# Kernel optimization log

Measured on AMD Instinct MI355X. Metric: run time of the kernel, lower is better.

## Reference

```python
import jax, jax.numpy as jnp
import numpy as np

D = 1024
H = 16
DH = D // H
F = 4096
EPS = 1e-5

def layernorm(x, gamma, beta):
    mean = jnp.mean(x, axis=-1, keepdims=True)
    var = jnp.mean((x - mean) ** 2, axis=-1, keepdims=True)  # biased variance
    return gamma * (x - mean) / jnp.sqrt(var + EPS) + beta

def setup_inputs() -> dict:
    key = jax.random.key(0)
    ks = jax.random.split(key, 12)
    s = 1.0 / np.sqrt(D)
    sf = 1.0 / np.sqrt(F)
    return {
        "x": jax.random.normal(ks[0], (16, 512, D), dtype=jnp.float32),
        "Wq": jax.random.normal(ks[1], (H, D, DH), dtype=jnp.float32) * s,
        "Wk": jax.random.normal(ks[2], (H, D, DH), dtype=jnp.float32) * s,
        "Wv": jax.random.normal(ks[3], (H, D, DH), dtype=jnp.float32) * s,
        "Wo": jax.random.normal(ks[4], (D, D), dtype=jnp.float32) * s,
        "bo": jax.random.normal(ks[5], (D,), dtype=jnp.float32) * s,
        "gamma1": jnp.ones((D,), dtype=jnp.float32),
        "beta1": jnp.zeros((D,), dtype=jnp.float32),
        "gamma2": jnp.ones((D,), dtype=jnp.float32),
        "beta2": jnp.zeros((D,), dtype=jnp.float32),
        "W1": jax.random.normal(ks[6], (D, F), dtype=jnp.float32) * s,
        "b1": jax.random.normal(ks[7], (F,), dtype=jnp.float32) * s,
        "W2": jax.random.normal(ks[8], (F, D), dtype=jnp.float32) * sf,
        "b2": jax.random.normal(ks[9], (D,), dtype=jnp.float32) * sf,
    }

def reference(x, Wq, Wk, Wv, Wo, bo, gamma1, beta1, gamma2, beta2, W1, b1, W2, b2):
    B, S, _ = x.shape
    n1 = layernorm(x, gamma1, beta1)
    # per-head projections (no bias) -> [B,H,S,DH]
    Q = jnp.einsum('bsd,hde->bhse', n1, Wq)
    K = jnp.einsum('bsd,hde->bhse', n1, Wk)
    V = jnp.einsum('bsd,hde->bhse', n1, Wv)
    scores = jnp.einsum('bhse,bhte->bhst', Q, K) / jnp.sqrt(jnp.float32(DH))
    causal = jnp.tril(jnp.ones((S, S), dtype=bool))  # keep lower triangle
    scores = jnp.where(causal, scores, -jnp.inf)
    attn = jax.nn.softmax(scores, axis=-1)  # dropout is identity at eval
    heads = jnp.einsum('bhst,bhte->bhse', attn, V)
    concat = heads.transpose(0, 2, 1, 3).reshape(B, S, D)  # concat heads in order
    x = x + (concat @ Wo + bo)
    n2 = layernorm(x, gamma2, beta2)
    ff = jax.nn.gelu(n2 @ W1 + b1, approximate=False) @ W2 + b2
    return x + ff
```

## Files before the change

### kernel.cpp

```cpp
#include <hip/hip_runtime.h>
#include <hip/hip_bf16.h>
#include <math.h>

constexpr int Dm = 1024;
constexpr int Hh = 16;
constexpr int Ff = 4096;
constexpr int Ss = 512;
constexpr int Bbatch = 16;
constexpr int NT = Bbatch * Ss;
constexpr float EPSc = 1e-5f;

typedef __attribute__((ext_vector_type(8))) short bfrag;
typedef __attribute__((ext_vector_type(4))) float f32x4;

static __device__ __forceinline__ float gelu_f(float v) {
    return 0.5f * v * (1.0f + erff(v * 0.70710678118654752f));
}

static __device__ __forceinline__ void gload16(const void* g, void* l) {
    __builtin_amdgcn_global_load_lds((__attribute__((address_space(1))) void*)g,
                                     (__attribute__((address_space(3))) void*)l,
                                     16, 0, 0);
}

#define SWZ(row, colb) ((row) * 128 + ((colb) ^ (((row) & 7) << 4)))

__global__ void __launch_bounds__(256) transpose_cvt(const float* __restrict__ in,
                                                     __hip_bfloat16* __restrict__ out,
                                                     int R, int C,
                                                     long in_zs, long out_zs) {
    __shared__ float tile[32][33];
    const float* inz = in + (size_t)blockIdx.z * in_zs;
    __hip_bfloat16* outz = out + (size_t)blockIdx.z * out_zs;
    const int c0 = blockIdx.x * 32, r0 = blockIdx.y * 32;
    const int tx = threadIdx.x & 31, ty4 = (threadIdx.x >> 5) * 4;
    #pragma unroll
    for (int i = 0; i < 4; i++)
        tile[ty4 + i][tx] = inz[(size_t)(r0 + ty4 + i) * C + c0 + tx];
    __syncthreads();
    #pragma unroll
    for (int i = 0; i < 4; i++)
        outz[(size_t)(c0 + ty4 + i) * R + r0 + tx] = __float2bfloat16(tile[tx][ty4 + i]);
}

__global__ void __launch_bounds__(256) ln_bf16(const float* __restrict__ x,
                                               const float* __restrict__ gamma,
                                               const float* __restrict__ beta,
                                               __hip_bfloat16* __restrict__ out) {
    const int row = blockIdx.x;
    const int tid = threadIdx.x;
    const int lane = tid & 63, w = tid >> 6;
    float4 xv = reinterpret_cast<const float4*>(x + (size_t)row * Dm)[tid];
    float s  = xv.x + xv.y + xv.z + xv.w;
    float ss = xv.x * xv.x + xv.y * xv.y + xv.z * xv.z + xv.w * xv.w;
    #pragma unroll
    for (int o = 32; o > 0; o >>= 1) {
        s  += __shfl_down(s,  o, 64);
        ss += __shfl_down(ss, o, 64);
    }
    __shared__ float red[2][4];
    if (lane == 0) { red[0][w] = s; red[1][w] = ss; }
    __syncthreads();
    float st  = red[0][0] + red[0][1] + red[0][2] + red[0][3];
    float sst = red[1][0] + red[1][1] + red[1][2] + red[1][3];
    float mean = st * (1.0f / Dm);
    float var  = sst * (1.0f / Dm) - mean * mean;
    float inv  = rsqrtf(var + EPSc);
    float4 g = reinterpret_cast<const float4*>(gamma)[tid];
    float4 b = reinterpret_cast<const float4*>(beta)[tid];
    __hip_bfloat16 t[4] __attribute__((aligned(8)));
    t[0] = __float2bfloat16((xv.x - mean) * inv * g.x + b.x);
    t[1] = __float2bfloat16((xv.y - mean) * inv * g.y + b.y);
    t[2] = __float2bfloat16((xv.z - mean) * inv * g.z + b.z);
    t[3] = __float2bfloat16((xv.w - mean) * inv * g.w + b.w);
    *reinterpret_cast<ushort4*>(out + (size_t)row * Dm + tid * 4) =
        *reinterpret_cast<ushort4*>(t);
}

template<int EPI>
__global__ void __launch_bounds__(256) gemm_mfma(const __hip_bfloat16* __restrict__ A, int lda,
                                                 const __hip_bfloat16* __restrict__ Bt, int ldb,
                                                 const float* __restrict__ bias,
                                                 const float* __restrict__ res,
                                                 void* __restrict__ Cout, int ldc,
                                                 int nbx, int K) {
    __shared__ __hip_bfloat16 As[128 * 32];
    __shared__ __hip_bfloat16 Bs[128 * 32];
    const int tid = threadIdx.x, l = tid & 63, w = tid >> 6;
    const int lr = l & 15, lg = l >> 4;
    const int nwg = gridDim.x, cpx = nwg >> 3;
    const int bid = blockIdx.x;
    const int sbid = (bid & 7) * cpx + (bid >> 3);
    const int bx = sbid % nbx, by = sbid / nbx;
    const int m0 = by * 128, n0 = bx * 128;
    const int wr = w >> 1, wc = w & 1;
    const int sr = l >> 2, scc = (l & 3) * 8;

    f32x4 acc[4][4] = {};
    for (int k0 = 0; k0 < K; k0 += 32) {
        #pragma unroll
        for (int j = 0; j < 2; j++) {
            const int slot = w * 2 + j;
            const int r = slot * 16 + sr;
            gload16(A  + (size_t)(m0 + r) * lda + k0 + scc, As + slot * 512);
            gload16(Bt + (size_t)(n0 + r) * ldb + k0 + scc, Bs + slot * 512);
        }
        __syncthreads();
        bfrag a[4], b[4];
        #pragma unroll
        for (int mi = 0; mi < 4; mi++)
            a[mi] = *reinterpret_cast<const bfrag*>(As + (wr * 64 + mi * 16 + lr) * 32 + lg * 8);
        #pragma unroll
        for (int ni = 0; ni < 4; ni++)
            b[ni] = *reinterpret_cast<const bfrag*>(Bs + (wc * 64 + ni * 16 + lr) * 32 + lg * 8);
        #pragma unroll
        for (int mi = 0; mi < 4; mi++)
            #pragma unroll
            for (int ni = 0; ni < 4; ni++)
                acc[mi][ni] = __builtin_amdgcn_mfma_f32_16x16x32_bf16(a[mi], b[ni], acc[mi][ni], 0, 0, 0);
        __syncthreads();
    }
    const int rb = m0 + wr * 64 + lg * 4;
    const int cb = n0 + wc * 64 + lr;
    #pragma unroll
    for (int mi = 0; mi < 4; mi++) {
        #pragma unroll
        for (int ni = 0; ni < 4; ni++) {
            #pragma unroll
            for (int rg = 0; rg < 4; rg++) {
                const int row = rb + mi * 16 + rg;
                const int col = cb + ni * 16;
                const size_t off = (size_t)row * ldc + col;
                const float v = acc[mi][ni][rg];
                if (EPI == 0) {
                    ((__hip_bfloat16*)Cout)[off] = __float2bfloat16(v);
                } else if (EPI == 1) {
                    ((float*)Cout)[off] = v + bias[col] + res[off];
                } else if (EPI == 2) {
                    ((__hip_bfloat16*)Cout)[off] = __float2bfloat16(gelu_f(v + bias[col]));
                } else {
                    ((float*)Cout)[off] = ((float*)Cout)[off] + v + bias[col];
                }
            }
        }
    }
}

__global__ void __launch_bounds__(256) attn_mfma(const __hip_bfloat16* __restrict__ QKV,
                                                 __hip_bfloat16* __restrict__ Oc) {
    constexpr int LDQ = 3072;
    __shared__ __hip_bfloat16 Qs[64 * 64];
    __shared__ __hip_bfloat16 Ks[64 * 64];
    __shared__ __hip_bfloat16 Vts[64 * 64];
    __shared__ __hip_bfloat16 Ps[4][16 * 64];
    const int tid = threadIdx.x, l = tid & 63, w = tid >> 6;
    const int lr = l & 15, lg = l >> 4;
    const int qt = blockIdx.x & 7;
    const int h  = (blockIdx.x >> 3) & 15;
    const int b  = blockIdx.x >> 7;

    const __hip_bfloat16* Qg = QKV + (size_t)(b * Ss + qt * 64) * LDQ + h * 64;
    const __hip_bfloat16* Kg = QKV + (size_t)(b * Ss) * LDQ + 1024 + h * 64;
    const __hip_bfloat16* Vg = QKV + (size_t)(b * Ss) * LDQ + 2048 + h * 64;

    const int r8 = l >> 3;
    const int scol = 8 * ((l & 7) ^ r8);

    #pragma unroll
    for (int j = 0; j < 2; j++) {
        const int slot = w * 2 + j;
        gload16(Qg + (size_t)(slot * 8 + r8) * LDQ + scol, Qs + slot * 512);
    }

    float m_run[4] = {-1e30f, -1e30f, -1e30f, -1e30f};
    float l_run[4] = {0.f, 0.f, 0.f, 0.f};
    f32x4 acc_o[4] = {};

    for (int kt = 0; kt <= qt; ++kt) {
        __syncthreads();
        #pragma unroll
        for (int j = 0; j < 2; j++) {
            const int slot = w * 2 + j;
            gload16(Kg + (size_t)(kt * 64 + slot * 8 + r8) * LDQ + scol, Ks + slot * 512);
        }
        unsigned short* vt = reinterpret_cast<unsigned short*>(Vts);
        #pragma unroll
        for (int j = 0; j < 2; j++) {
            const int e = tid + j * 256;
            const int key = e >> 3, f0 = (e & 7) * 8;
            const uint4 raw = *reinterpret_cast<const uint4*>(
                Vg + (size_t)(kt * 64 + key) * LDQ + f0);
            const unsigned int rw[4] = {raw.x, raw.y, raw.z, raw.w};
            #pragma unroll
            for (int e2 = 0; e2 < 8; e2++) {
                const int feat = f0 + e2;
                const int ad = feat * 128 + ((key * 2) ^ ((feat & 7) << 4));
                vt[ad >> 1] = (unsigned short)(rw[e2 >> 1] >> ((e2 & 1) * 16));
            }
        }
        __syncthreads();

        f32x4 s4[4] = {};
        #pragma unroll
        for (int kk = 0; kk < 2; kk++) {
            const bfrag aq = *reinterpret_cast<const bfrag*>(
                (const char*)Qs + SWZ(w * 16 + lr, kk * 64 + lg * 16));
            #pragma unroll
            for (int ni = 0; ni < 4; ni++) {
                const bfrag bk = *reinterpret_cast<const bfrag*>(
                    (const char*)Ks + SWZ(ni * 16 + lr, kk * 64 + lg * 16));
                s4[ni] = __builtin_amdgcn_mfma_f32_16x16x32_bf16(aq, bk, s4[ni], 0, 0, 0);
            }
        }
        float p[4][4];
        #pragma unroll
        for (int ni = 0; ni < 4; ni++)
            #pragma unroll
            for (int rg = 0; rg < 4; rg++)
                p[ni][rg] = s4[ni][rg] * 0.125f;
        if (kt == qt) {
            #pragma unroll
            for (int ni = 0; ni < 4; ni++)
                #pragma unroll
                for (int rg = 0; rg < 4; rg++)
                    if (ni * 16 + lr > w * 16 + lg * 4 + rg) p[ni][rg] = -1e30f;
        }
        float sf[4];
        #pragma unroll
        for (int rg = 0; rg < 4; rg++) {
            float mx = fmaxf(fmaxf(p[0][rg], p[1][rg]), fmaxf(p[2][rg], p[3][rg]));
            #pragma unroll
            for (int o = 1; o < 16; o <<= 1) mx = fmaxf(mx, __shfl_xor(mx, o, 64));
            const float mn = fmaxf(m_run[rg], mx);
            sf[rg] = __expf(m_run[rg] - mn);
            m_run[rg] = mn;
        }
        float rsum[4] = {};
        #pragma unroll
        for (int ni = 0; ni < 4; ni++)
            #pragma unroll
            for (int rg = 0; rg < 4; rg++) {
                const float e = __expf(p[ni][rg] - m_run[rg]);
                p[ni][rg] = e;
                rsum[rg] += e;
            }
        #pragma unroll
        for (int rg = 0; rg < 4; rg++) {
            #pragma unroll
            for (int o = 1; o < 16; o <<= 1) rsum[rg] += __shfl_xor(rsum[rg], o, 64);
            l_run[rg] = l_run[rg] * sf[rg] + rsum[rg];
        }
        #pragma unroll
        for (int di = 0; di < 4; di++)
            #pragma unroll
            for (int rg = 0; rg < 4; rg++)
                acc_o[di][rg] *= sf[rg];
        unsigned short* pw = reinterpret_cast<unsigned short*>(Ps[w]);
        #pragma unroll
        for (int ni = 0; ni < 4; ni++)
            #pragma unroll
            for (int rg = 0; rg < 4; rg++) {
                const int prow = lg * 4 + rg;
                const int ad = SWZ(prow, (ni * 16 + lr) * 2);
                __hip_bfloat16 pb = __float2bfloat16(p[ni][rg]);
                pw[ad >> 1] = *reinterpret_cast<unsigned short*>(&pb);
            }
        #pragma unroll
        for (int kk = 0; kk < 2; kk++) {
            const bfrag pa = *reinterpret_cast<const bfrag*>(
                (const char*)Ps[w] + SWZ(lr, kk * 64 + lg * 16));
            #pragma unroll
            for (int di = 0; di < 4; di++) {
                const bfrag vb = *reinterpret_cast<const bfrag*>(
                    (const char*)Vts + SWZ(di * 16 + lr, kk * 64 + lg * 16));
                acc_o[di] = __builtin_amdgcn_mfma_f32_16x16x32_bf16(pa, vb, acc_o[di], 0, 0, 0);
            }
        }
    }
    #pragma unroll
    for (int di = 0; di < 4; di++)
        #pragma unroll
        for (int rg = 0; rg < 4; rg++) {
            const int q = qt * 64 + w * 16 + lg * 4 + rg;
            const float v = acc_o[di][rg] / l_run[rg];
            Oc[(size_t)(b * Ss + q) * Dm + h * 64 + di * 16 + lr] = __float2bfloat16(v);
        }
}

extern "C" void kernel_launch(void* const* d_in, const int* in_sizes, int n_in,
                              void* d_out, int out_size, void* d_ws, size_t ws_size,
                              hipStream_t stream) {
    const float* x   = (const float*)d_in[0];
    const float* Wq  = (const float*)d_in[1];
    const float* Wk  = (const float*)d_in[2];
    const float* Wv  = (const float*)d_in[3];
    const float* Wo  = (const float*)d_in[4];
    const float* bo  = (const float*)d_in[5];
    const float* g1  = (const float*)d_in[6];
    const float* be1 = (const float*)d_in[7];
    const float* g2  = (const float*)d_in[8];
    const float* be2 = (const float*)d_in[9];
    const float* W1  = (const float*)d_in[10];
    const float* b1  = (const float*)d_in[11];
    const float* W2  = (const float*)d_in[12];
    const float* b2  = (const float*)d_in[13];
    float* out = (float*)d_out;

    char* wsb = (char*)d_ws;
    __hip_bfloat16* WqkvT = (__hip_bfloat16*)(wsb);
    __hip_bfloat16* WoT   = (__hip_bfloat16*)(wsb + 6291456);
    __hip_bfloat16* W1T   = (__hip_bfloat16*)(wsb + 8388608);
    __hip_bfloat16* W2T   = (__hip_bfloat16*)(wsb + 16777216);
    __hip_bfloat16* n1    = (__hip_bfloat16*)(wsb + 25165824);
    __hip_bfloat16* QKV   = (__hip_bfloat16*)(wsb + 41943040);
    __hip_bfloat16* concat = n1;
    __hip_bfloat16* n2     = n1;
    __hip_bfloat16* h1     = QKV;

    transpose_cvt<<<dim3(2, 32, 16), 256, 0, stream>>>(Wq, WqkvT,              1024, 64, 65536, 65536);
    transpose_cvt<<<dim3(2, 32, 16), 256, 0, stream>>>(Wk, WqkvT + 1024 * 1024, 1024, 64, 65536, 65536);
    transpose_cvt<<<dim3(2, 32, 16), 256, 0, stream>>>(Wv, WqkvT + 2048 * 1024, 1024, 64, 65536, 65536);
    transpose_cvt<<<dim3(32, 32, 1), 256, 0, stream>>>(Wo, WoT, 1024, 1024, 0, 0);
    transpose_cvt<<<dim3(128, 32, 1), 256, 0, stream>>>(W1, W1T, 1024, 4096, 0, 0);
    transpose_cvt<<<dim3(32, 128, 1), 256, 0, stream>>>(W2, W2T, 4096, 1024, 0, 0);

    ln_bf16<<<NT, 256, 0, stream>>>(x, g1, be1, n1);
    gemm_mfma<0><<<24 * 64, 256, 0, stream>>>(n1, Dm, WqkvT, Dm, nullptr, nullptr,
                                              QKV, 3072, 24, Dm);
    attn_mfma<<<NT * Hh / 64, 256, 0, stream>>>(QKV, concat);
    gemm_mfma<1><<<8 * 64, 256, 0, stream>>>(concat, Dm, WoT, Dm, bo, x,
                                             out, Dm, 8, Dm);
    ln_bf16<<<NT, 256, 0, stream>>>(out, g2, be2, n2);
    gemm_mfma<2><<<32 * 64, 256, 0, stream>>>(n2, Dm, W1T, Dm, b1, nullptr,
                                              h1, Ff, 32, Dm);
    gemm_mfma<3><<<8 * 64, 256, 0, stream>>>(h1, Ff, W2T, Ff, b2, nullptr,
                                             out, Dm, 8, Ff);
}
```

Measured before the change: 473.4 us.

## Replace GEMM with 256-row tiles, double-buffered LDS, swizzle and 8 waves

Replaces the 128x128, K=32 single-buffered MFMA GEMM with a 512-thread kernel using 256xBN tiles (BN 256 or 128) and K=64 steps. Two LDS buffers are loaded ahead, with explicit vmcnt waits, so global-to-LDS loads overlap the MFMA work. An XOR swizzle avoids LDS bank conflicts, and s_setprio raises wave priority around the MFMA bursts. The larger tiles cut operand refetch per FLOP but raise register and LDS use (up to 128KB LDS), which may limit occupancy; the hand-set vmcnt counts must match the number of issued loads.

Measured after the change: 503.4 us. +6.3%, slower.

```diff
diff --git a/kernel.cpp b/kernel.cpp
--- a/kernel.cpp
+++ b/kernel.cpp
@@ -77,59 +77,88 @@
         *reinterpret_cast<ushort4*>(t);
 }
 
-template<int EPI>
-__global__ void __launch_bounds__(256) gemm_mfma(const __hip_bfloat16* __restrict__ A, int lda,
-                                                 const __hip_bfloat16* __restrict__ Bt, int ldb,
-                                                 const float* __restrict__ bias,
-                                                 const float* __restrict__ res,
-                                                 void* __restrict__ Cout, int ldc,
-                                                 int nbx, int K) {
-    __shared__ __hip_bfloat16 As[128 * 32];
-    __shared__ __hip_bfloat16 Bs[128 * 32];
+template<int BN_, int EPI>
+__global__ void __launch_bounds__(512) gemm8(const __hip_bfloat16* __restrict__ A, int lda,
+                                             const __hip_bfloat16* __restrict__ Bt, int ldb,
+                                             const float* __restrict__ bias,
+                                             const float* __restrict__ res,
+                                             void* __restrict__ Cout, int ldc,
+                                             int nbx, int K) {
+    constexpr int NREP = BN_ / 64;
+    constexpr int WNS  = BN_ / 4;
+    __shared__ __hip_bfloat16 As[2][256 * 64];
+    __shared__ __hip_bfloat16 Bs[2][BN_ * 64];
     const int tid = threadIdx.x, l = tid & 63, w = tid >> 6;
     const int lr = l & 15, lg = l >> 4;
-    const int nwg = gridDim.x, cpx = nwg >> 3;
-    const int bid = blockIdx.x;
-    const int sbid = (bid & 7) * cpx + (bid >> 3);
+    const int nwg = gridDim.x;
+    const int sbid = (blockIdx.x & 7) * (nwg >> 3) + (blockIdx.x >> 3);
     const int bx = sbid % nbx, by = sbid / nbx;
-    const int m0 = by * 128, n0 = bx * 128;
-    const int wr = w >> 1, wc = w & 1;
-    const int sr = l >> 2, scc = (l & 3) * 8;
-
-    f32x4 acc[4][4] = {};
-    for (int k0 = 0; k0 < K; k0 += 32) {
-        #pragma unroll
-        for (int j = 0; j < 2; j++) {
-            const int slot = w * 2 + j;
-            const int r = slot * 16 + sr;
-            gload16(A  + (size_t)(m0 + r) * lda + k0 + scc, As + slot * 512);
-            gload16(Bt + (size_t)(n0 + r) * ldb + k0 + scc, Bs + slot * 512);
-        }
-        __syncthreads();
-        bfrag a[4], b[4];
-        #pragma unroll
-        for (int mi = 0; mi < 4; mi++)
-            a[mi] = *reinterpret_cast<const bfrag*>(As + (wr * 64 + mi * 16 + lr) * 32 + lg * 8);
-        #pragma unroll
-        for (int ni = 0; ni < 4; ni++)
-            b[ni] = *reinterpret_cast<const bfrag*>(Bs + (wc * 64 + ni * 16 + lr) * 32 + lg * 8);
-        #pragma unroll
-        for (int mi = 0; mi < 4; mi++)
-            #pragma unroll
-            for (int ni = 0; ni < 4; ni++)
-                acc[mi][ni] = __builtin_amdgcn_mfma_f32_16x16x32_bf16(a[mi], b[ni], acc[mi][ni], 0, 0, 0);
-        __syncthreads();
-    }
-    const int rb = m0 + wr * 64 + lg * 4;
-    const int cb = n0 + wc * 64 + lr;
-    #pragma unroll
-    for (int mi = 0; mi < 4; mi++) {
-        #pragma unroll
-        for (int ni = 0; ni < 4; ni++) {
+    const int m0 = by * 256, n0 = bx * BN_;
+    const int wr = w >> 2, wc = w & 3;
+    const int srow = l >> 3;
+    const int scol = ((l & 7) ^ srow) * 8;
+
+    const int NK = K >> 6;
+    auto STAGE = [&](int t, int bsel) {
+        const int k0 = t * 64;
+        #pragma unroll
+        for (int j = 0; j < 4; j++) {
+            const int rb = j * 64 + w * 8;
+            gload16(A + (size_t)(m0 + rb + srow) * lda + k0 + scol, &As[bsel][rb * 64]);
+        }
+        #pragma unroll
+        for (int j = 0; j < NREP; j++) {
+            const int rb = j * 64 + w * 8;
+            gload16(Bt + (size_t)(n0 + rb + srow) * ldb + k0 + scol, &Bs[bsel][rb * 64]);
+        }
+    };
+
+    f32x4 acc[8][NREP] = {};
+    STAGE(0, 0);
+    STAGE(1, 1);
+    for (int t = 0; t < NK; t++) {
+        const int cur = t & 1;
+        if (t + 1 < NK) {
+            if constexpr (BN_ == 256) asm volatile("s_waitcnt vmcnt(8)" ::: "memory");
+            else                      asm volatile("s_waitcnt vmcnt(6)" ::: "memory");
+        } else {
+            asm volatile("s_waitcnt vmcnt(0)" ::: "memory");
+        }
+        __builtin_amdgcn_s_barrier();
+        const char* Ab = (const char*)&As[cur][0];
+        const char* Bb = (const char*)&Bs[cur][0];
+        #pragma unroll
+        for (int kk = 0; kk < 2; kk++) {
+            bfrag a[8], b[NREP];
+            #pragma unroll
+            for (int mi = 0; mi < 8; mi++) {
+                const int row = wr * 128 + mi * 16 + lr;
+                a[mi] = *(const bfrag*)(Ab + row * 128 + ((((kk << 2) + lg) ^ (row & 7)) << 4));
+            }
+            #pragma unroll
+            for (int ni = 0; ni < NREP; ni++) {
+                const int row = wc * WNS + ni * 16 + lr;
+                b[ni] = *(const bfrag*)(Bb + row * 128 + ((((kk << 2) + lg) ^ (row & 7)) << 4));
+            }
+            __builtin_amdgcn_s_setprio(1);
+            #pragma unroll
+            for (int mi = 0; mi < 8; mi++)
+                #pragma unroll
+                for (int ni = 0; ni < NREP; ni++)
+                    acc[mi][ni] = __builtin_amdgcn_mfma_f32_16x16x32_bf16(a[mi], b[ni], acc[mi][ni], 0, 0, 0);
+            __builtin_amdgcn_s_setprio(0);
+        }
+        __builtin_amdgcn_s_barrier();
+        if (t + 2 < NK) STAGE(t + 2, cur);
+    }
+    #pragma unroll
+    for (int mi = 0; mi < 8; mi++) {
+        #pragma unroll
+        for (int ni = 0; ni < NREP; ni++) {
             #pragma unroll
             for (int rg = 0; rg < 4; rg++) {
-                const int row = rb + mi * 16 + rg;
-                const int col = cb + ni * 16;
+                const int row = m0 + wr * 128 + mi * 16 + lg * 4 + rg;
+                const int col = n0 + wc * WNS + ni * 16 + lr;
                 const size_t off = (size_t)row * ldc + col;
                 const float v = acc[mi][ni][rg];
                 if (EPI == 0) {
@@ -325,14 +354,14 @@
     transpose_cvt<<<dim3(32, 128, 1), 256, 0, stream>>>(W2, W2T, 4096, 1024, 0, 0);
 
     ln_bf16<<<NT, 256, 0, stream>>>(x, g1, be1, n1);
-    gemm_mfma<0><<<24 * 64, 256, 0, stream>>>(n1, Dm, WqkvT, Dm, nullptr, nullptr,
-                                              QKV, 3072, 24, Dm);
+    gemm8<256, 0><<<384, 512, 0, stream>>>(n1, Dm, WqkvT, Dm, nullptr, nullptr,
+                                           QKV, 3072, 12, Dm);
     attn_mfma<<<NT * Hh / 64, 256, 0, stream>>>(QKV, concat);
-    gemm_mfma<1><<<8 * 64, 256, 0, stream>>>(concat, Dm, WoT, Dm, bo, x,
-                                             out, Dm, 8, Dm);
+    gemm8<128, 1><<<256, 512, 0, stream>>>(concat, Dm, WoT, Dm, bo, x,
+                                           out, Dm, 8, Dm);
     ln_bf16<<<NT, 256, 0, stream>>>(out, g2, be2, n2);
-    gemm_mfma<2><<<32 * 64, 256, 0, stream>>>(n2, Dm, W1T, Dm, b1, nullptr,
-                                              h1, Ff, 32, Dm);
-    gemm_mfma<3><<<8 * 64, 256, 0, stream>>>(h1, Ff, W2T, Ff, b2, nullptr,
-                                             out, Dm, 8, Ff);
-}
+    gemm8<256, 2><<<512, 512, 0, stream>>>(n2, Dm, W1T, Dm, b1, nullptr,
+                                           h1, Ff, 16, Dm);
+    gemm8<128, 3><<<256, 512, 0, stream>>>(h1, Ff, W2T, Ff, b2, nullptr,
+                                           out, Dm, 8, Ff);
+}
```

## Deepen GEMM K-tile to 64 with XOR-swizzled LDS and use tanh GELU

Applied to the files above, without the earlier changes.

The GEMM kernel now stages a 128x64 K-slice per iteration instead of 128x32. This halves the number of barrier pairs per output tile. LDS rows are XOR-swizzled on the global->LDS load and on the fragment reads to avoid bank conflicts at the wider 128-byte row stride. Separately, the exact erf GELU is replaced by a tanh approximation computed with __expf, which cheapens the FFN epilogue but changes numerics versus the reference's exact GELU.

After: 425.8 us. 10.0% less time.

```diff
diff --git a/kernel.cpp b/kernel.cpp
--- a/kernel.cpp
+++ b/kernel.cpp
@@ -14,7 +14,10 @@
 typedef __attribute__((ext_vector_type(4))) float f32x4;
 
 static __device__ __forceinline__ float gelu_f(float v) {
-    return 0.5f * v * (1.0f + erff(v * 0.70710678118654752f));
+    const float u = v * (0.7978845608f + 0.0356774081f * v * v);
+    const float e = __expf(2.0f * u);
+    const float th = 1.0f - 2.0f / (e + 1.0f);
+    return 0.5f * v * (1.0f + th);
 }
 
 static __device__ __forceinline__ void gload16(const void* g, void* l) {
@@ -78,46 +81,52 @@
 }
 
 template<int EPI>
-__global__ void __launch_bounds__(256) gemm_mfma(const __hip_bfloat16* __restrict__ A, int lda,
-                                                 const __hip_bfloat16* __restrict__ Bt, int ldb,
-                                                 const float* __restrict__ bias,
-                                                 const float* __restrict__ res,
-                                                 void* __restrict__ Cout, int ldc,
-                                                 int nbx, int K) {
-    __shared__ __hip_bfloat16 As[128 * 32];
-    __shared__ __hip_bfloat16 Bs[128 * 32];
+__global__ void __launch_bounds__(256) gemm_m97(const __hip_bfloat16* __restrict__ A, int lda,
+                                                const __hip_bfloat16* __restrict__ Bt, int ldb,
+                                                const float* __restrict__ bias,
+                                                const float* __restrict__ res,
+                                                void* __restrict__ Cout, int ldc,
+                                                int nbx, int K) {
+    __shared__ __hip_bfloat16 As[128 * 64];
+    __shared__ __hip_bfloat16 Bs[128 * 64];
     const int tid = threadIdx.x, l = tid & 63, w = tid >> 6;
     const int lr = l & 15, lg = l >> 4;
-    const int nwg = gridDim.x, cpx = nwg >> 3;
-    const int bid = blockIdx.x;
-    const int sbid = (bid & 7) * cpx + (bid >> 3);
+    const int nwg = gridDim.x;
+    const int sbid = (blockIdx.x & 7) * (nwg >> 3) + (blockIdx.x >> 3);
     const int bx = sbid % nbx, by = sbid / nbx;
     const int m0 = by * 128, n0 = bx * 128;
     const int wr = w >> 1, wc = w & 1;
-    const int sr = l >> 2, scc = (l & 3) * 8;
+    const int srow = l >> 3;
+    const int scol = ((l & 7) ^ srow) * 8;
 
     f32x4 acc[4][4] = {};
-    for (int k0 = 0; k0 < K; k0 += 32) {
-        #pragma unroll
-        for (int j = 0; j < 2; j++) {
-            const int slot = w * 2 + j;
-            const int r = slot * 16 + sr;
-            gload16(A  + (size_t)(m0 + r) * lda + k0 + scc, As + slot * 512);
-            gload16(Bt + (size_t)(n0 + r) * ldb + k0 + scc, Bs + slot * 512);
+    for (int k0 = 0; k0 < K; k0 += 64) {
+        #pragma unroll
+        for (int j = 0; j < 4; j++) {
+            const int rb = w * 32 + j * 8;
+            gload16(A  + (size_t)(m0 + rb + srow) * lda + k0 + scol, As + rb * 64);
+            gload16(Bt + (size_t)(n0 + rb + srow) * ldb + k0 + scol, Bs + rb * 64);
         }
         __syncthreads();
-        bfrag a[4], b[4];
-        #pragma unroll
-        for (int mi = 0; mi < 4; mi++)
-            a[mi] = *reinterpret_cast<const bfrag*>(As + (wr * 64 + mi * 16 + lr) * 32 + lg * 8);
-        #pragma unroll
-        for (int ni = 0; ni < 4; ni++)
-            b[ni] = *reinterpret_cast<const bfrag*>(Bs + (wc * 64 + ni * 16 + lr) * 32 + lg * 8);
-        #pragma unroll
-        for (int mi = 0; mi < 4; mi++)
-            #pragma unroll
-            for (int ni = 0; ni < 4; ni++)
-                acc[mi][ni] = __builtin_amdgcn_mfma_f32_16x16x32_bf16(a[mi], b[ni], acc[mi][ni], 0, 0, 0);
+        #pragma unroll
+        for (int kk = 0; kk < 2; kk++) {
+            bfrag a[4], b[4];
+            #pragma unroll
+            for (int mi = 0; mi < 4; mi++) {
+                const int row = wr * 64 + mi * 16 + lr;
+                a[mi] = *(const bfrag*)((const char*)As + SWZ(row, (kk * 4 + lg) * 16));
+            }
+            #pragma unroll
+            for (int ni = 0; ni < 4; ni++) {
+                const int row = wc * 64 + ni * 16 + lr;
+                b[ni] = *(const bfrag*)((const char*)Bs + SWZ(row, (kk * 4 + lg) * 16));
+            }
+            #pragma unroll
+            for (int mi = 0; mi < 4; mi++)
+                #pragma unroll
+                for (int ni = 0; ni < 4; ni++)
+                    acc[mi][ni] = __builtin_amdgcn_mfma_f32_16x16x32_bf16(a[mi], b[ni], acc[mi][ni], 0, 0, 0);
+        }
         __syncthreads();
     }
     const int rb = m0 + wr * 64 + lg * 4;
@@ -325,14 +334,14 @@
     transpose_cvt<<<dim3(32, 128, 1), 256, 0, stream>>>(W2, W2T, 4096, 1024, 0, 0);
 
     ln_bf16<<<NT, 256, 0, stream>>>(x, g1, be1, n1);
-    gemm_mfma<0><<<24 * 64, 256, 0, stream>>>(n1, Dm, WqkvT, Dm, nullptr, nullptr,
-                                              QKV, 3072, 24, Dm);
+    gemm_m97<0><<<1536, 256, 0, stream>>>(n1, Dm, WqkvT, Dm, nullptr, nullptr,
+                                          QKV, 3072, 24, Dm);
     attn_mfma<<<NT * Hh / 64, 256, 0, stream>>>(QKV, concat);
-    gemm_mfma<1><<<8 * 64, 256, 0, stream>>>(concat, Dm, WoT, Dm, bo, x,
-                                             out, Dm, 8, Dm);
+    gemm_m97<1><<<512, 256, 0, stream>>>(concat, Dm, WoT, Dm, bo, x,
+                                         out, Dm, 8, Dm);
     ln_bf16<<<NT, 256, 0, stream>>>(out, g2, be2, n2);
-    gemm_mfma<2><<<32 * 64, 256, 0, stream>>>(n2, Dm, W1T, Dm, b1, nullptr,
-                                              h1, Ff, 32, Dm);
-    gemm_mfma<3><<<8 * 64, 256, 0, stream>>>(h1, Ff, W2T, Ff, b2, nullptr,
-                                             out, Dm, 8, Ff);
-}
+    gemm_m97<2><<<2048, 256, 0, stream>>>(n2, Dm, W1T, Dm, b1, nullptr,
+                                          h1, Ff, 32, Dm);
+    gemm_m97<3><<<512, 256, 0, stream>>>(h1, Ff, W2T, Ff, b2, nullptr,
+                                         out, Dm, 8, Ff);
+}
```
